# Optimization experiments

Hardware: AMD Instinct MI355X
Metric: run time of the kernel (lower is better)

The kernel has to match this reference:

```python
import jax, jax.numpy as jnp
import numpy as np

VOCAB, E, VD, B, S, W = 50000, 300, 128, 32, 64, 30
NEG = 1e12


def setup_inputs() -> dict:
    key = jax.random.key(0)
    ks = jax.random.split(key, 8)
    emb_table = jax.random.normal(ks[0], (VOCAB, E), jnp.float32) * 0.02
    emb_table = emb_table.at[0].set(0.0)  # padding_idx=0 row is zeros
    W1 = jax.random.normal(ks[1], (VD, 32), jnp.float32) * (1.0 / np.sqrt(VD))
    b1 = jnp.zeros((32,), jnp.float32)
    W2 = jax.random.normal(ks[2], (2 * E, E), jnp.float32) * (1.0 / np.sqrt(2 * E))
    b2 = jnp.zeros((E,), jnp.float32)
    word_idx = jax.random.randint(ks[3], (B, S, W), 0, VOCAB, jnp.int32)
    voice_embeded = jax.random.normal(ks[4], (B, S, VD), jnp.float32)
    sent_nums = jax.random.randint(ks[5], (B,), 1, S + 1, jnp.int32)
    return {"word_idx": word_idx, "voice_embeded": voice_embeded,
            "sent_nums": sent_nums, "max_sent_nums": S,
            "emb_table": emb_table, "W1": W1, "b1": b1, "W2": W2, "b2": b2}


def reference(word_idx, voice_embeded, sent_nums, max_sent_nums, emb_table, W1, b1, W2, b2):
    # sequence mask over sentence dim: [B, S]
    m = (jnp.arange(max_sent_nums)[None, :] < sent_nums[:, None]).astype(jnp.float32)
    word_embeded = emb_table[word_idx]                     # [B, S, W, E]
    Q = voice_embeded @ W1 + b1                            # [B, S, 32]
    K = voice_embeded @ W1 + b1                            # same dense1 weights
    A = jnp.einsum('bqd,bkd->bqk', Q, K)                   # [B, S, S]
    # additive mask applied on key axis (transpose -> add mask -> transpose back)
    A = A - (1.0 - m)[:, None, :] * NEG
    A = jax.nn.softmax(A, axis=-1)                         # voice_A
    V = word_embeded.reshape(B, max_sent_nums, -1)         # [B, S, W*E]
    O = jnp.einsum('bqk,bkd->bqd', A, V)                   # [B, S, W*E]
    O = O * m[:, :, None]                                  # multiplicative mask
    O = O.reshape(B, max_sent_nums, W, E)                  # [B, S, W, E]
    O = jnp.concatenate([O, word_embeded], axis=-1)        # [B, S, W, 2E]
    O = O @ W2 + b2                                        # [B, S, W, E]
    # transpose(1,3) then transpose(2,3): [B,S,W,E] -> [B,E,S,W]
    O = jnp.transpose(O, (0, 3, 1, 2))
    return O, A
```

## Files before the change

### kernel.cpp

```cpp
#include <hip/hip_runtime.h>

#define BB 32
#define SS 64
#define WW 30
#define EE 300
#define VDD 128
#define HH 32

typedef short bf16x8 __attribute__((ext_vector_type(8)));
typedef float f32x4 __attribute__((ext_vector_type(4)));

__device__ __forceinline__ ushort f2bf(float f) {
  union { float f; unsigned u; } x; x.f = f;
  unsigned r = x.u + 0x7fffu + ((x.u >> 16) & 1u);
  return (ushort)(r >> 16);
}
__device__ __forceinline__ float bf2f(ushort u) {
  union { unsigned u; float f; } x; x.u = ((unsigned)u) << 16; return x.f;
}

__global__ __launch_bounds__(256) void k_front(
    const float* __restrict__ voice, const int* __restrict__ sent,
    const float* __restrict__ W1, const float* __restrict__ b1,
    const int* __restrict__ widx, const float* __restrict__ emb,
    const float* __restrict__ W2,
    float* __restrict__ Aout, ushort* __restrict__ web, ushort* __restrict__ w2tp) {
  __shared__ float sq[SS][33];
  int blk = blockIdx.x, t = threadIdx.x;
  if (blk < 32) {
    int b = blk;
    for (int o = t; o < SS * HH; o += 256) {
      int s = o >> 5, j = o & 31;
      const float* vrow = voice + ((size_t)b * SS + s) * VDD;
      float acc = b1[j];
      #pragma unroll 8
      for (int d = 0; d < VDD; ++d) acc += vrow[d] * W1[d * HH + j];
      sq[s][j] = acc;
    }
    __syncthreads();
    int sn = sent[b];
    int wv = t >> 6, ln = t & 63;
    for (int q = wv; q < SS; q += 4) {
      float acc = 0.f;
      #pragma unroll
      for (int j = 0; j < HH; ++j) acc += sq[q][j] * sq[ln][j];
      if (ln >= sn) acc -= 1e12f;
      float mx = acc;
      #pragma unroll
      for (int off = 32; off; off >>= 1) mx = fmaxf(mx, __shfl_xor(mx, off));
      float e = expf(acc - mx);
      float sm = e;
      #pragma unroll
      for (int off = 32; off; off >>= 1) sm += __shfl_xor(sm, off);
      Aout[((size_t)b * SS + q) * SS + ln] = e / sm;
    }
  } else if (blk < 127) {
    int g = (blk - 32) * 256 + t;
    if (g < 380 * 64) {
      int tI = g >> 6, lane = g & 63;
      int kc2 = tI / 19, ms = tI - kc2 * 19;
      int kc = kc2 >> 1, ks = kc2 & 1;
      int lg = lane >> 4, lr = lane & 15;
      int e = ms * 16 + lr;
      int kp0 = kc * 64 + ks * 32 + lg * 8;
      ushort v[8];
      #pragma unroll
      for (int j = 0; j < 8; ++j) {
        int kp = kp0 + j;
        int c = kp < 320 ? kp : kp - 20;
        bool ok = (e < EE) && (kp < 320 ? kp < 300 : kp < 620);
        v[j] = ok ? f2bf(W2[(size_t)c * EE + e]) : (ushort)0;
      }
      ushort* dst = w2tp + (size_t)g * 8;
      *(ushort4*)dst = *(ushort4*)&v[0];
      *(ushort4*)(dst + 4) = *(ushort4*)&v[4];
    }
  } else {
    int tid = (blk - 127) * 256 + t;
    if (tid < BB * SS * WW * 75) {
      int row = tid / 75, p = tid - row * 75;
      int idx = widx[row];
      float4 v = *(const float4*)(emb + (size_t)idx * EE + p * 4);
      ushort4 o;
      o.x = f2bf(v.x); o.y = f2bf(v.y); o.z = f2bf(v.z); o.w = f2bf(v.w);
      *(ushort4*)(web + (size_t)row * EE + p * 4) = o;
    }
  }
}

__global__ __launch_bounds__(256) void k_pv2(
    const float* __restrict__ Aout, const ushort* __restrict__ web,
    const int* __restrict__ sent, ushort* __restrict__ obf) {
  __shared__ ushort sa[64][72];
  __shared__ ushort vt[256][72];
  int nc = blockIdx.x, b = blockIdx.y, t = threadIdx.x;
  int n0blk = nc * 256;
  for (int i = t; i < 64 * 16; i += 256) {
    int q = i >> 4, c4 = (i & 15) << 2;
    float4 f = *(const float4*)(Aout + (size_t)b * 4096 + q * 64 + c4);
    ushort4 u; u.x = f2bf(f.x); u.y = f2bf(f.y); u.z = f2bf(f.z); u.w = f2bf(f.w);
    *(ushort4*)&sa[q][c4] = u;
  }
  int kk = t >> 5, nl0 = (t & 31) << 3;
  int swz = (t & 31) & 7;
  for (int p = 0; p < 8; ++p) {
    int k = p * 8 + kk;
    int n = n0blk + nl0;
    ushort v[8];
    if (n + 7 < 9000) {
      const ushort* s = web + (size_t)(b * 64 + k) * 9000 + n;
      *(ushort4*)&v[0] = *(const ushort4*)s;
      *(ushort4*)&v[4] = *(const ushort4*)(s + 4);
    } else {
      #pragma unroll
      for (int j = 0; j < 8; ++j) v[j] = 0;
    }
    int c = (((k >> 3) ^ swz) << 3) + (k & 7);
    #pragma unroll
    for (int j = 0; j < 8; ++j) vt[nl0 + j][c] = v[j];
  }
  __syncthreads();
  int sn = sent[b];
  int wv = t >> 6, ln = t & 63, lr = ln & 15, lg = ln >> 4;
  int nbase = wv * 64;
  f32x4 acc[4][4];
  #pragma unroll
  for (int mt = 0; mt < 4; ++mt)
    #pragma unroll
    for (int nf = 0; nf < 4; ++nf) acc[mt][nf] = (f32x4){0.f, 0.f, 0.f, 0.f};
  #pragma unroll
  for (int ks = 0; ks < 2; ++ks) {
    if (ks * 32 < sn) {
      bf16x8 bfrag[4];
      #pragma unroll
      for (int nf = 0; nf < 4; ++nf) {
        int row = nbase + nf * 16 + lr;
        int gp = (ks * 4 + lg) ^ ((row >> 3) & 7);
        bfrag[nf] = *(const bf16x8*)&vt[row][gp << 3];
      }
      #pragma unroll
      for (int mt = 0; mt < 4; ++mt) {
        if (mt * 16 < sn) {
          bf16x8 afrag = *(const bf16x8*)&sa[mt * 16 + lr][ks * 32 + lg * 8];
          #pragma unroll
          for (int nf = 0; nf < 4; ++nf)
            acc[mt][nf] = __builtin_amdgcn_mfma_f32_16x16x32_bf16(
                afrag, bfrag[nf], acc[mt][nf], 0, 0, 0);
        }
      }
    }
  }
  #pragma unroll
  for (int mt = 0; mt < 4; ++mt) {
    #pragma unroll
    for (int nf = 0; nf < 4; ++nf) {
      int n = n0blk + nbase + nf * 16 + lr;
      if (n < 9000) {
        #pragma unroll
        for (int j = 0; j < 4; ++j) {
          int q = mt * 16 + lg * 4 + j;
          obf[(size_t)(b * 64 + q) * 9000 + n] =
              (q < sn) ? f2bf(acc[mt][nf][j]) : (ushort)0;
        }
      }
    }
  }
}

__global__ __launch_bounds__(512, 4) void k_out4(
    const ushort* __restrict__ obf, const ushort* __restrict__ web,
    const ushort* __restrict__ w2tp, const float* __restrict__ b2,
    float* __restrict__ out) {
  __shared__ ushort sb[64][324];
  __shared__ float sb2[304];
  int blk = blockIdx.x, t = threadIdx.x;
  int wv = t >> 6, ln = t & 63;
  size_t r0 = (size_t)blk * 64;
  int bbat = blk / 30;
  int rin0 = (blk % 30) * 64;
  for (int i = t; i < 304; i += 512) sb2[i] = (i < 300) ? b2[i] : 0.f;
  f32x4 acc[3][4];
  #pragma unroll
  for (int i = 0; i < 3; ++i)
    #pragma unroll
    for (int nf = 0; nf < 4; ++nf) acc[i][nf] = (f32x4){0.f, 0.f, 0.f, 0.f};
  int lr = ln & 15, lg = ln >> 4;

  for (int ph = 0; ph < 2; ++ph) {
    const ushort* src = ph ? web : obf;
    for (int i = t; i < 64 * 40; i += 512) {
      int row = i / 40, c8 = (i - row * 40) * 8;
      ushort4 lo = {0, 0, 0, 0}, hi = {0, 0, 0, 0};
      const ushort* s = src + (r0 + row) * 300 + c8;
      if (c8 + 8 <= 300) {
        lo = *(const ushort4*)s;
        hi = *(const ushort4*)(s + 4);
      } else if (c8 < 300) {
        lo = *(const ushort4*)s;
      }
      *(ushort4*)&sb[row][c8] = lo;
      *(ushort4*)&sb[row][c8 + 4] = hi;
    }
    __syncthreads();
    #pragma unroll
    for (int kc = 0; kc < 5; ++kc) {
      bf16x8 bfr[4][2];
      #pragma unroll
      for (int nf = 0; nf < 4; ++nf)
        #pragma unroll
        for (int ks = 0; ks < 2; ++ks)
          bfr[nf][ks] = *(const bf16x8*)&sb[nf * 16 + lr][kc * 64 + ks * 32 + lg * 8];
      #pragma unroll
      for (int i = 0; i < 3; ++i) {
        int ms = wv + 8 * i;
        if (ms < 19) {
          #pragma unroll
          for (int ks = 0; ks < 2; ++ks) {
            bf16x8 afr = *(const bf16x8*)(w2tp +
                ((size_t)(((ph * 5 + kc) * 2 + ks) * 19 + ms) * 64 + ln) * 8);
            #pragma unroll
            for (int nf = 0; nf < 4; ++nf)
              acc[i][nf] = __builtin_amdgcn_mfma_f32_16x16x32_bf16(
                  afr, bfr[nf][ks], acc[i][nf], 0, 0, 0);
          }
        }
      }
    }
    __syncthreads();
  }
  #pragma unroll
  for (int i = 0; i < 3; ++i) {
    int ms = wv + 8 * i;
    if (ms >= 19) continue;
    #pragma unroll
    for (int nf = 0; nf < 4; ++nf) {
      int rin = rin0 + nf * 16 + lr;
      #pragma unroll
      for (int j = 0; j < 4; ++j) {
        int e = ms * 16 + lg * 4 + j;
        if (e < 300)
          out[(size_t)(bbat * 300 + e) * 1920 + rin] = acc[i][nf][j] + sb2[e];
      }
    }
  }
}

extern "C" void kernel_launch(void* const* d_in, const int* in_sizes, int n_in,
                              void* d_out, int out_size, void* d_ws, size_t ws_size,
                              hipStream_t stream) {
  const int*   widx  = (const int*)d_in[0];
  const float* voice = (const float*)d_in[1];
  const int*   sent  = (const int*)d_in[2];
  const float* emb   = (const float*)d_in[4];
  const float* W1    = (const float*)d_in[5];
  const float* b1    = (const float*)d_in[6];
  const float* W2    = (const float*)d_in[7];
  const float* b2    = (const float*)d_in[8];
  float* out  = (float*)d_out;
  float* Aout = out + (size_t)BB * EE * SS * WW;

  ushort* web  = (ushort*)d_ws;
  ushort* obf  = web + (size_t)18432000;
  ushort* w2tp = obf + (size_t)18432000;

  hipLaunchKernelGGL(k_front, dim3(18127), dim3(256), 0, stream,
                     voice, sent, W1, b1, widx, emb, W2, Aout, web, w2tp);
  hipLaunchKernelGGL(k_pv2, dim3(36, BB), dim3(256), 0, stream, Aout, web, sent, obf);
  hipLaunchKernelGGL(k_out4, dim3(960), dim3(512), 0, stream, obf, web, w2tp, b2, out);
}
```

Measured before the change: 122.3 us.

## Pre-convert embedding table to bf16 and skip masked rows in output GEMM

```diff
diff --git a/kernel.cpp b/kernel.cpp
--- a/kernel.cpp
+++ b/kernel.cpp
@@ -15,16 +15,15 @@
   unsigned r = x.u + 0x7fffu + ((x.u >> 16) & 1u);
   return (ushort)(r >> 16);
 }
-__device__ __forceinline__ float bf2f(ushort u) {
-  union { unsigned u; float f; } x; x.u = ((unsigned)u) << 16; return x.f;
-}
-
-__global__ __launch_bounds__(256) void k_front(
+
+#define CONV_PIECES 3750000
+#define CONV_BLOCKS 14649
+
+__global__ __launch_bounds__(256) void k_front2(
     const float* __restrict__ voice, const int* __restrict__ sent,
     const float* __restrict__ W1, const float* __restrict__ b1,
-    const int* __restrict__ widx, const float* __restrict__ emb,
-    const float* __restrict__ W2,
-    float* __restrict__ Aout, ushort* __restrict__ web, ushort* __restrict__ w2tp) {
+    const float* __restrict__ emb, const float* __restrict__ W2,
+    float* __restrict__ Aout, ushort* __restrict__ emb16, ushort* __restrict__ w2tp) {
   __shared__ float sq[SS][33];
   int blk = blockIdx.x, t = threadIdx.x;
   if (blk < 32) {
@@ -76,19 +75,28 @@
       *(ushort4*)(dst + 4) = *(ushort4*)&v[4];
     }
   } else {
-    int tid = (blk - 127) * 256 + t;
-    if (tid < BB * SS * WW * 75) {
-      int row = tid / 75, p = tid - row * 75;
-      int idx = widx[row];
-      float4 v = *(const float4*)(emb + (size_t)idx * EE + p * 4);
+    int g = (blk - 127) * 256 + t;
+    if (g < CONV_PIECES) {
+      float4 v = *(const float4*)(emb + (size_t)g * 4);
       ushort4 o;
       o.x = f2bf(v.x); o.y = f2bf(v.y); o.z = f2bf(v.z); o.w = f2bf(v.w);
-      *(ushort4*)(web + (size_t)row * EE + p * 4) = o;
-    }
-  }
-}
-
-__global__ __launch_bounds__(256) void k_pv2(
+      *(ushort4*)(emb16 + (size_t)g * 4) = o;
+    }
+  }
+}
+
+__global__ __launch_bounds__(256) void k_gather2(
+    const int* __restrict__ widx, const ushort* __restrict__ emb16,
+    ushort* __restrict__ web) {
+  int tid = blockIdx.x * 256 + threadIdx.x;
+  if (tid >= BB * SS * WW * 75) return;
+  int row = tid / 75, p = tid - row * 75;
+  int idx = widx[row];
+  ushort4 v = *(const ushort4*)(emb16 + (size_t)idx * EE + p * 4);
+  *(ushort4*)(web + (size_t)row * EE + p * 4) = v;
+}
+
+__global__ __launch_bounds__(256) void k_pv3(
     const float* __restrict__ Aout, const ushort* __restrict__ web,
     const int* __restrict__ sent, ushort* __restrict__ obf) {
   __shared__ ushort sa[64][72];
@@ -159,18 +167,18 @@
         #pragma unroll
         for (int j = 0; j < 4; ++j) {
           int q = mt * 16 + lg * 4 + j;
-          obf[(size_t)(b * 64 + q) * 9000 + n] =
-              (q < sn) ? f2bf(acc[mt][nf][j]) : (ushort)0;
-        }
-      }
-    }
-  }
-}
-
-__global__ __launch_bounds__(512, 4) void k_out4(
+          if (q < sn)
+            obf[(size_t)(b * 64 + q) * 9000 + n] = f2bf(acc[mt][nf][j]);
+        }
+      }
+    }
+  }
+}
+
+__global__ __launch_bounds__(512, 4) void k_out6(
     const ushort* __restrict__ obf, const ushort* __restrict__ web,
     const ushort* __restrict__ w2tp, const float* __restrict__ b2,
-    float* __restrict__ out) {
+    const int* __restrict__ sent, float* __restrict__ out) {
   __shared__ ushort sb[64][324];
   __shared__ float sb2[304];
   int blk = blockIdx.x, t = threadIdx.x;
@@ -178,6 +186,8 @@
   size_t r0 = (size_t)blk * 64;
   int bbat = blk / 30;
   int rin0 = (blk % 30) * 64;
+  int sn = sent[bbat];
+  int liveN = sn * 30 - rin0; liveN = liveN < 0 ? 0 : (liveN > 64 ? 64 : liveN);
   for (int i = t; i < 304; i += 512) sb2[i] = (i < 300) ? b2[i] : 0.f;
   f32x4 acc[3][4];
   #pragma unroll
@@ -188,28 +198,33 @@
 
   for (int ph = 0; ph < 2; ++ph) {
     const ushort* src = ph ? web : obf;
+    int rowsLive = ph ? 64 : liveN;
     for (int i = t; i < 64 * 40; i += 512) {
       int row = i / 40, c8 = (i - row * 40) * 8;
       ushort4 lo = {0, 0, 0, 0}, hi = {0, 0, 0, 0};
-      const ushort* s = src + (r0 + row) * 300 + c8;
-      if (c8 + 8 <= 300) {
-        lo = *(const ushort4*)s;
-        hi = *(const ushort4*)(s + 4);
-      } else if (c8 < 300) {
-        lo = *(const ushort4*)s;
+      if (row < rowsLive) {
+        const ushort* s = src + (r0 + row) * 300 + c8;
+        if (c8 + 8 <= 300) {
+          lo = *(const ushort4*)s;
+          hi = *(const ushort4*)(s + 4);
+        } else if (c8 < 300) {
+          lo = *(const ushort4*)s;
+        }
       }
       *(ushort4*)&sb[row][c8] = lo;
       *(ushort4*)&sb[row][c8 + 4] = hi;
     }
     __syncthreads();
+    int nfLive = (rowsLive + 15) >> 4;
     #pragma unroll
     for (int kc = 0; kc < 5; ++kc) {
       bf16x8 bfr[4][2];
       #pragma unroll
       for (int nf = 0; nf < 4; ++nf)
-        #pragma unroll
-        for (int ks = 0; ks < 2; ++ks)
-          bfr[nf][ks] = *(const bf16x8*)&sb[nf * 16 + lr][kc * 64 + ks * 32 + lg * 8];
+        if (nf < nfLive)
+          #pragma unroll
+          for (int ks = 0; ks < 2; ++ks)
+            bfr[nf][ks] = *(const bf16x8*)&sb[nf * 16 + lr][kc * 64 + ks * 32 + lg * 8];
       #pragma unroll
       for (int i = 0; i < 3; ++i) {
         int ms = wv + 8 * i;
@@ -220,8 +235,9 @@
                 ((size_t)(((ph * 5 + kc) * 2 + ks) * 19 + ms) * 64 + ln) * 8);
             #pragma unroll
             for (int nf = 0; nf < 4; ++nf)
-              acc[i][nf] = __builtin_amdgcn_mfma_f32_16x16x32_bf16(
-                  afr, bfr[nf][ks], acc[i][nf], 0, 0, 0);
+              if (nf < nfLive)
+                acc[i][nf] = __builtin_amdgcn_mfma_f32_16x16x32_bf16(
+                    afr, bfr[nf][ks], acc[i][nf], 0, 0, 0);
           }
         }
       }
@@ -259,12 +275,14 @@
   float* out  = (float*)d_out;
   float* Aout = out + (size_t)BB * EE * SS * WW;
 
-  ushort* web  = (ushort*)d_ws;
-  ushort* obf  = web + (size_t)18432000;
-  ushort* w2tp = obf + (size_t)18432000;
-
-  hipLaunchKernelGGL(k_front, dim3(18127), dim3(256), 0, stream,
-                     voice, sent, W1, b1, widx, emb, W2, Aout, web, w2tp);
-  hipLaunchKernelGGL(k_pv2, dim3(36, BB), dim3(256), 0, stream, Aout, web, sent, obf);
-  hipLaunchKernelGGL(k_out4, dim3(960), dim3(512), 0, stream, obf, web, w2tp, b2, out);
-}
+  ushort* web   = (ushort*)d_ws;
+  ushort* obf   = web + (size_t)18432000;
+  ushort* emb16 = obf;
+  ushort* w2tp  = obf + (size_t)18432000;
+
+  hipLaunchKernelGGL(k_front2, dim3(127 + CONV_BLOCKS), dim3(256), 0, stream,
+                     voice, sent, W1, b1, emb, W2, Aout, emb16, w2tp);
+  hipLaunchKernelGGL(k_gather2, dim3(18000), dim3(256), 0, stream, widx, emb16, web);
+  hipLaunchKernelGGL(k_pv3, dim3(36, BB), dim3(256), 0, stream, Aout, web, sent, obf);
+  hipLaunchKernelGGL(k_out6, dim3(960), dim3(512), 0, stream, obf, web, w2tp, b2, sent, out);
+}
```

New measurement: 127.2 us. 1.04x slower.
